# Kernel optimization log

Measured on AMD Instinct MI355X. Metric: run time of the kernel, lower is better.

The kernel has to match this reference:

```python
import jax, jax.numpy as jnp
import numpy as np

T, D, H, C, MAXLEN = 1024, 512, 512, 50257, 150


def setup_inputs() -> dict:
    key = jax.random.key(0)
    ks = iter(jax.random.split(key, 32))
    s = 0.1  # keep gates out of saturation
    def p(shape):
        return jax.random.normal(next(ks), shape, jnp.float32) * s
    return {
        "x": jax.random.normal(next(ks), (T, D), jnp.float32),
        "enc_Wih0": p((2, 4 * H, D)), "enc_Whh0": p((2, 4 * H, H)), "enc_b0": p((2, 4 * H)),
        "enc_Wih1": p((2, 4 * H, 2 * H)), "enc_Whh1": p((2, 4 * H, H)), "enc_b1": p((2, 4 * H)),
        "dec_Wih0": p((2, 4 * H, D)), "dec_Whh0": p((2, 4 * H, H)), "dec_b0": p((2, 4 * H)),
        "dec_Wih1": p((2, 4 * H, 2 * H)), "dec_Whh1": p((2, 4 * H, H)), "dec_b1": p((2, 4 * H)),
        "lin_W": p((C, 2 * H)), "lin_b": p((C,)),
        "emb": p((C, D)),
        "bos": p((D,)),
        "out_max_len": MAXLEN,
    }


def _cell(x, h, c, Wih, Whh, b):
    # PyTorch LSTM gate order: i, f, g, o; b = b_ih + b_hh
    g = Wih @ x + Whh @ h + b
    i, f, gg, o = jnp.split(g, 4)
    c = jax.nn.sigmoid(f) * c + jax.nn.sigmoid(i) * jnp.tanh(gg)
    h = jax.nn.sigmoid(o) * jnp.tanh(c)
    return h, c


def _run_dir(xs, Wih, Whh, b, reverse):
    Hh = Whh.shape[1]
    init = (jnp.zeros((Hh,), xs.dtype), jnp.zeros((Hh,), xs.dtype))
    def step(carry, xt):
        h, c = carry
        h, c = _cell(xt, h, c, Wih, Whh, b)
        return (h, c), h
    (hT, cT), hs = jax.lax.scan(step, init, xs, reverse=reverse)
    return hs, hT, cT  # hs aligned with input order


def _encode(x, layers):
    xs = x  # [T, D]
    h_fin, c_fin = [], []
    for (Wih, Whh, b) in layers:
        hs_f, hf, cf = _run_dir(xs, Wih[0], Whh[0], b[0], False)
        hs_b, hb, cb = _run_dir(xs, Wih[1], Whh[1], b[1], True)
        xs = jnp.concatenate([hs_f, hs_b], axis=-1)  # [T, 2H]
        h_fin.append(jnp.stack([hf, hb]))
        c_fin.append(jnp.stack([cf, cb]))
    return jnp.stack(h_fin), jnp.stack(c_fin)  # [L, 2, H]


def reference(x, enc_Wih0, enc_Whh0, enc_b0, enc_Wih1, enc_Whh1, enc_b1,
              dec_Wih0, dec_Whh0, dec_b0, dec_Wih1, dec_Whh1, dec_b1,
              lin_W, lin_b, emb, bos, out_max_len):
    layers_enc = [(enc_Wih0, enc_Whh0, enc_b0), (enc_Wih1, enc_Whh1, enc_b1)]
    layers_dec = [(dec_Wih0, dec_Whh0, dec_b0), (dec_Wih1, dec_Whh1, dec_b1)]

    h, c = _encode(x, layers_enc)  # [2, 2, H] each

    def dec_step(carry, _):
        buf, h, c = carry
        inp = buf
        nh, nc = [], []
        for l, (Wih, Whh, b) in enumerate(layers_dec):
            hf, cf = _cell(inp, h[l, 0], c[l, 0], Wih[0], Whh[0], b[0])
            hb, cb = _cell(inp, h[l, 1], c[l, 1], Wih[1], Whh[1], b[1])
            inp = jnp.concatenate([hf, hb])  # [2H]
            nh.append(jnp.stack([hf, hb]))
            nc.append(jnp.stack([cf, cb]))
        logits = lin_W @ inp + lin_b          # [C]
        tok = jnp.argmax(logits)              # greedy feedback
        buf = emb[tok]                        # [D]
        return (buf, jnp.stack(nh), jnp.stack(nc)), (logits, tok)

    _, (logits_seq, toks) = jax.lax.scan(dec_step, (bos, h, c), None, length=out_max_len)
    return logits_seq, toks  # [L_out, C], [L_out]
```

## Files before the change

### kernel.cpp

```cpp
#include <hip/hip_runtime.h>

typedef unsigned int u32;
typedef unsigned short u16;
typedef unsigned long long u64;

#define DEV static __device__ __forceinline__

DEV float sigf(float x){ return 1.0f / (1.0f + expf(-x)); }

DEV u64  ldA64(const u64* p){ return __hip_atomic_load(p, __ATOMIC_RELAXED, __HIP_MEMORY_SCOPE_AGENT); }
DEV void stA64(u64* p, u64 v){ __hip_atomic_store(p, v, __ATOMIC_RELAXED, __HIP_MEMORY_SCOPE_AGENT); }
DEV float ldAf(const float* p){ return __hip_atomic_load(p, __ATOMIC_RELAXED, __HIP_MEMORY_SCOPE_AGENT); }
DEV void stAf(float* p, float v){ __hip_atomic_store(p, v, __ATOMIC_RELAXED, __HIP_MEMORY_SCOPE_AGENT); }
DEV u32  ldA32(const u32* p){ return __hip_atomic_load(p, __ATOMIC_RELAXED, __HIP_MEMORY_SCOPE_AGENT); }

DEV u64 packHV(float h, u32 tag){ return (((u64)__float_as_uint(h)) << 32) | (u64)tag; }
DEV float unpackH(u64 v){ return __uint_as_float((u32)(v >> 32)); }

DEV u64 packKeyT(float v, u32 row, u32 tagv){
  u32 u = __float_as_uint(v);
  u = (u & 0x80000000u) ? ~u : (u | 0x80000000u);
  return (((u64)u) << 32) | ((u64)(0x1FFFFu - row) << 15) | (u64)tagv;
}
DEV float unpackKeyF(u64 k){
  u32 u = (u32)(k >> 32);
  u = (u & 0x80000000u) ? (u ^ 0x80000000u) : ~u;
  return __uint_as_float(u);
}

#if defined(__has_builtin)
#if __has_builtin(__builtin_amdgcn_sdot4)
#define HAVE_SDOT4 1
#endif
#endif
DEV int dot4i8(u32 a, u32 b, int acc){
#ifdef HAVE_SDOT4
  return __builtin_amdgcn_sdot4((int)a, (int)b, acc, false);
#else
  int s = acc;
  s += ((int)(a << 24) >> 24) * ((int)(b << 24) >> 24);
  s += ((int)(a << 16) >> 24) * ((int)(b << 16) >> 24);
  s += ((int)(a <<  8) >> 24) * ((int)(b <<  8) >> 24);
  s += ((int)(a      ) >> 24) * ((int)(b      ) >> 24);
  return s;
#endif
}

DEV int q8c(float v){ int q = (int)rintf(v); return q < -127 ? -127 : (q > 127 ? 127 : q); }
DEV u32 pk4(int a, int b, int c, int d){
  return (u32)(a & 255) | ((u32)(b & 255) << 8) | ((u32)(c & 255) << 16) | ((u32)(d & 255) << 24);
}

DEV float dotrow(const float4 A, const float4 B, const float4 Cc, const float4 D,
                 const float4 q0, const float4 q1, const float4 q2, const float4 q3){
  float s;
  s  = A.x*q0.x + A.y*q0.y + A.z*q0.z + A.w*q0.w;
  s += B.x*q1.x + B.y*q1.y + B.z*q1.z + B.w*q1.w;
  s += Cc.x*q2.x + Cc.y*q2.y + Cc.z*q2.z + Cc.w*q2.w;
  s += D.x*q3.x + D.y*q3.y + D.z*q3.z + D.w*q3.w;
  return s;
}

struct SM {
  float w1s[24576];
  float inpP[1600];
  float linp[1024];
  u32   qhp[256];
  float srow[200];
  float erow[200];
  float red[8];
  float dots[16];
  float cst0[4];
  float cst1[4];
  u64   wkey[4];
};

template<int CPT> DEV int pidx(int c){ int b = c / CPT; return b * (CPT + 4) + (c - b * CPT); }

template<int CPT, int DIN>
DEV void loadw(float* wreg, const float* Wih, const float* Whh, int jb4){
  const int tid = threadIdx.x, r = tid >> 4, p = tid & 15;
  const int R = 512 * (r >> 2) + jb4 + (r & 3);
  const float* s1 = Wih + (size_t)R * DIN;
  const float* s2 = Whh + (size_t)R * 512;
  #pragma unroll
  for (int k = 0; k < CPT; k += 4){
    const int col = p * CPT + k;
    const float4 v = *(const float4*)((col < DIN) ? (s1 + col) : (s2 + col - DIN));
    wreg[k] = v.x; wreg[k+1] = v.y; wreg[k+2] = v.z; wreg[k+3] = v.w;
  }
}

template<int CPT, int DIN, bool LOW>
DEV float dotp_reg(const float* wreg, const float* inpP, float acc){
  const int p = threadIdx.x & 15;
  const float* xi = inpP + p * (CPT + 4);
  #pragma unroll
  for (int k = 0; k < CPT; k += 4){
    const int col = p * CPT + k;
    if ((col < DIN) == LOW){
      const float4 xv = *(const float4*)(xi + k);
      acc = fmaf(wreg[k],   xv.x, acc);
      acc = fmaf(wreg[k+1], xv.y, acc);
      acc = fmaf(wreg[k+2], xv.z, acc);
      acc = fmaf(wreg[k+3], xv.w, acc);
    }
  }
  return acc;
}
DEV void dred16(float acc, float* dots){
  #pragma unroll
  for (int s = 1; s < 16; s <<= 1) acc += __shfl_xor(acc, s, 64);
  if ((threadIdx.x & 15) == 0) dots[threadIdx.x >> 4] = acc;
}

template<int CPT>
DEV void dot16(const float* wreg, const float* inpP, float* dots){
  const int tid = threadIdx.x, p = tid & 15;
  const float* xi = inpP + p * (CPT + 4);
  float acc = 0.f;
  #pragma unroll
  for (int k = 0; k < CPT; k += 4){
    const float4 xv = *(const float4*)(xi + k);
    acc = fmaf(wreg[k],   xv.x, acc);
    acc = fmaf(wreg[k+1], xv.y, acc);
    acc = fmaf(wreg[k+2], xv.z, acc);
    acc = fmaf(wreg[k+3], xv.w, acc);
  }
  dred16(acc, dots);
}

DEV void dot16_w1(const float* w1s, const float* inpP, float* dots){
  const int tid = threadIdx.x, p = tid & 15;
  const float* xi = inpP + p * 100;
  float acc = 0.f;
  #pragma unroll
  for (int k = 0; k < 96; k += 4){
    const float4 w4 = *(const float4*)(w1s + (k >> 2) * 1024 + tid * 4);
    const float4 xv = *(const float4*)(xi + k);
    acc = fmaf(w4.x, xv.x, acc);
    acc = fmaf(w4.y, xv.y, acc);
    acc = fmaf(w4.z, xv.z, acc);
    acc = fmaf(w4.w, xv.w, acc);
  }
  dred16(acc, dots);
}

DEV void gbar_phase(u32* g, u32 ev){
  __syncthreads();
  if (threadIdx.x == 0){
    __hip_atomic_fetch_add(g, 1u, __ATOMIC_RELEASE, __HIP_MEMORY_SCOPE_AGENT);
    const u32 tgt = 256u * ev;
    while (ldA32(g) < tgt) __builtin_amdgcn_s_sleep(8);
    (void)__hip_atomic_fetch_add(g, 0u, __ATOMIC_ACQUIRE, __HIP_MEMORY_SCOPE_AGENT);
    asm volatile("" ::: "memory");
  }
  __syncthreads();
}

DEV u64 exchange(u64* slots, u64 kwave , int w, u32 tagv, SM& sm){
  const int tid = threadIdx.x;
  if ((tid & 63) == 0) sm.wkey[tid >> 6] = kwave;
  __syncthreads();
  if (tid == 0){
    u64 k4 = sm.wkey[0];
    if (sm.wkey[1] > k4) k4 = sm.wkey[1];
    if (sm.wkey[2] > k4) k4 = sm.wkey[2];
    if (sm.wkey[3] > k4) k4 = sm.wkey[3];
    stA64(slots + (size_t)w * 16, k4);
  }
  __syncthreads();
  const u64* p = slots + (size_t)tid * 16;
  u64 kv = ldA64(p);
  while ((u32)(kv & 0x7FFFu) != tagv){ __builtin_amdgcn_s_sleep(1); kv = ldA64(p); }
  #pragma unroll
  for (int s = 1; s < 64; s <<= 1){
    const u64 o = (u64)__shfl_xor((unsigned long long)kv, s, 64);
    if (o > kv) kv = o;
  }
  if ((tid & 63) == 0) sm.wkey[tid >> 6] = kv;
  __syncthreads();
  u64 gk = sm.wkey[0];
  if (sm.wkey[1] > gk) gk = sm.wkey[1];
  if (sm.wkey[2] > gk) gk = sm.wkey[2];
  if (sm.wkey[3] > gk) gk = sm.wkey[3];
  return gk;
}

template<int DIN, bool WRITE_XS>
DEV void enc_layer(const float* __restrict__ xg, float* __restrict__ xs_out,
                   const float* __restrict__ Wih, const float* __restrict__ Whh,
                   const float* __restrict__ bias,
                   u64* __restrict__ ht, float* __restrict__ hfinL, float* __restrict__ cfinL,
                   const int dir, const int jb4, SM& sm)
{
  constexpr int CPT = (DIN + 512) / 16;
  constexpr int NX  = DIN / 256;
  const int tid = threadIdx.x;
  float wreg[CPT];
  loadw<CPT, DIN>(wreg, Wih + (size_t)dir * 2048 * DIN, Whh + (size_t)dir * 2048 * 512, jb4);
  float b_i = 0.f, b_f = 0.f, b_g = 0.f, b_o = 0.f;
  if (tid < 4){
    const int j = jb4 + tid;
    sm.cst0[tid] = 0.f;
    b_i = bias[dir*2048 +        j];
    b_f = bias[dir*2048 +  512 + j];
    b_g = bias[dir*2048 + 1024 + j];
    b_o = bias[dir*2048 + 1536 + j];
  }
  float xr[NX];
  {
    const int t0 = dir ? 1023 : 0;
    #pragma unroll
    for (int i = 0; i < NX; ++i){
      const int c = tid + 256 * i;
      xr[i] = (DIN == 512) ? xg[(size_t)t0 * DIN + c] : ldAf(xg + (size_t)t0 * DIN + c);
    }
  }
  for (int step = 0; step < 1024; ++step){
    #pragma unroll
    for (int i = 0; i < NX; ++i) sm.inpP[pidx<CPT>(tid + 256 * i)] = xr[i];
    __syncthreads();
    const u64* hp = ht + (step & 1) * 512;
    const u32 want = (u32)step;
    u64 a = ldA64(hp + tid*2);
    u64 b = ldA64(hp + tid*2 + 1);
    float acc = dotp_reg<CPT, DIN, true>(wreg, sm.inpP, 0.f);
    while ((u32)a != want){ __builtin_amdgcn_s_sleep(1); a = ldA64(hp + tid*2); }
    while ((u32)b != want){ __builtin_amdgcn_s_sleep(1); b = ldA64(hp + tid*2 + 1); }
    sm.inpP[pidx<CPT>(DIN + tid*2)]     = unpackH(a);
    sm.inpP[pidx<CPT>(DIN + tid*2 + 1)] = unpackH(b);
    __syncthreads();
    if (step < 1023){
      const int tn = dir ? (1022 - step) : (step + 1);
      #pragma unroll
      for (int i = 0; i < NX; ++i){
        const int c = tid + 256 * i;
        xr[i] = (DIN == 512) ? xg[(size_t)tn * DIN + c] : ldAf(xg + (size_t)tn * DIN + c);
      }
    }
    acc = dotp_reg<CPT, DIN, false>(wreg, sm.inpP, acc);
    dred16(acc, sm.dots);
    __syncthreads();
    if (tid < 4){
      const float gi = sm.dots[tid]      + b_i;
      const float gf = sm.dots[4 + tid]  + b_f;
      const float gg = sm.dots[8 + tid]  + b_g;
      const float go = sm.dots[12 + tid] + b_o;
      const float cc = sigf(gf) * sm.cst0[tid] + sigf(gi) * tanhf(gg);
      const float hh = sigf(go) * tanhf(cc);
      sm.cst0[tid] = cc;
      const int t = dir ? (1023 - step) : step;
      const int j = jb4 + tid;
      stA64(ht + ((step + 1) & 1) * 512 + j, packHV(hh, (u32)(step + 1)));
      if (WRITE_XS) stAf(xs_out + (size_t)t * 1024 + dir * 512 + j, hh);
      if (step == 1023){ stAf(hfinL + dir*512 + j, hh); stAf(cfinL + dir*512 + j, cc); }
    }
  }
}

__global__ void bilstm_init(u32* ws){
  for (u32 i = threadIdx.x; i < 49152u; i += 256u) ws[i] = 0u;
}

__global__ void cvt_q8(const float* __restrict__ w, uint4* __restrict__ q8,
                       float* __restrict__ meta, const int C){
  const int wv = threadIdx.x >> 6, lane = threadIdx.x & 63;
  const int stride = gridDim.x * 4;
  for (int r = blockIdx.x * 4 + wv; r < C; r += stride){
    const float4* src = (const float4*)(w + (size_t)r * 1024) + lane * 4;
    const float4 v0 = src[0], v1 = src[1], v2 = src[2], v3 = src[3];
    float m = fmaxf(fmaxf(fmaxf(fabsf(v0.x), fabsf(v0.y)), fmaxf(fabsf(v0.z), fabsf(v0.w))),
                    fmaxf(fmaxf(fabsf(v1.x), fabsf(v1.y)), fmaxf(fabsf(v1.z), fabsf(v1.w))));
    m = fmaxf(m, fmaxf(fmaxf(fabsf(v2.x), fabsf(v2.y)), fmaxf(fabsf(v2.z), fabsf(v2.w))));
    m = fmaxf(m, fmaxf(fmaxf(fabsf(v3.x), fabsf(v3.y)), fmaxf(fabsf(v3.z), fabsf(v3.w))));
    #pragma unroll
    for (int s = 1; s < 64; s <<= 1) m = fmaxf(m, __shfl_xor(m, s, 64));
    const float inv = (m > 1e-30f) ? (127.0f / m) : 0.0f;
    const float sw = m * (1.0f / 127.0f);
    const int qa0 = q8c(v0.x*inv), qa1 = q8c(v0.y*inv), qa2 = q8c(v0.z*inv), qa3 = q8c(v0.w*inv);
    const int qb0 = q8c(v1.x*inv), qb1 = q8c(v1.y*inv), qb2 = q8c(v1.z*inv), qb3 = q8c(v1.w*inv);
    const int qc0 = q8c(v2.x*inv), qc1 = q8c(v2.y*inv), qc2 = q8c(v2.z*inv), qc3 = q8c(v2.w*inv);
    const int qd0 = q8c(v3.x*inv), qd1 = q8c(v3.y*inv), qd2 = q8c(v3.z*inv), qd3 = q8c(v3.w*inv);
    uint4 st;
    st.x = pk4(qa0,qa1,qa2,qa3); st.y = pk4(qb0,qb1,qb2,qb3);
    st.z = pk4(qc0,qc1,qc2,qc3); st.w = pk4(qd0,qd1,qd2,qd3);
    q8[(size_t)r * 64 + lane] = st;
    float sq = (float)(abs(qa0)+abs(qa1)+abs(qa2)+abs(qa3)+abs(qb0)+abs(qb1)+abs(qb2)+abs(qb3)
                     + abs(qc0)+abs(qc1)+abs(qc2)+abs(qc3)+abs(qd0)+abs(qd1)+abs(qd2)+abs(qd3));
    #pragma unroll
    for (int s = 1; s < 64; s <<= 1) sq += __shfl_xor(sq, s, 64);
    if (lane == 0){ meta[2*r] = sw; meta[2*r+1] = sq; }
  }
}

template<int LINQ8>
__global__ __launch_bounds__(256, 1)
void bilstm_persist(const float* __restrict__ x,
                    const float* __restrict__ eW0, const float* __restrict__ eU0, const float* __restrict__ eb0,
                    const float* __restrict__ eW1, const float* __restrict__ eU1, const float* __restrict__ eb1,
                    const float* __restrict__ dW0, const float* __restrict__ dU0, const float* __restrict__ db0,
                    const float* __restrict__ dW1, const float* __restrict__ dU1, const float* __restrict__ db1,
                    const float* __restrict__ linW, const float* __restrict__ linb,
                    const float* __restrict__ emb, const float* __restrict__ bos,
                    float* __restrict__ out, float* __restrict__ ws, const int L, const int C)
{
  __shared__ SM sm;
  const int w = blockIdx.x;
  const int tid = threadIdx.x;
  const int dir = (w >> 2) & 1;
  const int jb4 = ((w >> 3) * 4 + (w & 3)) * 4;

  u64*  htagE = (u64*)ws;
  u64*  h0t   = htagE + 4096;
  u64*  h1t   = h0t + 2048;
  float* hfin = (float*)(h1t + 2048);
  float* cfin = hfin + 2048;
  u32*  gbar  = (u32*)(cfin + 2048);
  u64*  gkeyA = (u64*)((char*)ws + 131072);
  u64*  gkeyB = (u64*)((char*)ws + 163840);
  const float* meta = (const float*)((const char*)ws + 196608);
  const uint4* q8u  = (const uint4*)((const char*)ws + 602112);
  float* xs1  = out;

  enc_layer<512,  true >(x,   xs1,     eW0, eU0, eb0, htagE + (0*2 + dir)*1024, hfin,        cfin,        dir, jb4, sm);
  gbar_phase(gbar, 1);
  enc_layer<1024, false>(xs1, nullptr, eW1, eU1, eb1, htagE + (1*2 + dir)*1024, hfin + 1024, cfin + 1024, dir, jb4, sm);
  gbar_phase(gbar, 2);

  float w0reg[64];
  loadw<64, 512>(w0reg, dW0 + (size_t)dir*2048*512, dU0 + (size_t)dir*2048*512, jb4);
  {
    const int r = tid >> 4, p = tid & 15;
    const int R = 512 * (r >> 2) + jb4 + (r & 3);
    const float* s1 = dW1 + (size_t)dir*2048*1024 + (size_t)R * 1024;
    const float* s2 = dU1 + (size_t)dir*2048*512  + (size_t)R * 512;
    #pragma unroll
    for (int k = 0; k < 96; k += 4){
      const int col = p * 96 + k;
      const float4 v = *(const float4*)((col < 1024) ? (s1 + col) : (s2 + col - 1024));
      *(float4*)(sm.w1s + (k >> 2) * 1024 + tid * 4) = v;
    }
  }

  float b0i=0,b0f=0,b0g=0,b0o=0, b1i=0,b1f=0,b1g=0,b1o=0;
  if (tid < 4){
    const int j = jb4 + tid;
    sm.cst0[tid] = ldAf(&cfin[dir*512 + j]);
    sm.cst1[tid] = ldAf(&cfin[1024 + dir*512 + j]);
    b0i = db0[dir*2048 + j];        b0f = db0[dir*2048 + 512 + j];
    b0g = db0[dir*2048 + 1024 + j]; b0o = db0[dir*2048 + 1536 + j];
    b1i = db1[dir*2048 + j];        b1f = db1[dir*2048 + 512 + j];
    b1g = db1[dir*2048 + 1024 + j]; b1o = db1[dir*2048 + 1536 + j];
  }
  const int rbase = w * 196 + (w < 81 ? w : 81);
  const int rn    = 196 + (w < 81 ? 1 : 0);
  int tok = 0;

  for (int t = 0; t < L; ++t){
    {
      const float* src = (t == 0) ? bos : (emb + (size_t)tok * 512);
      sm.inpP[pidx<64>(tid)]       = src[tid];
      sm.inpP[pidx<64>(tid + 256)] = src[tid + 256];
      if (t == 0){
        sm.inpP[pidx<64>(512 + tid*2)]     = ldAf(&hfin[dir*512 + tid*2]);
        sm.inpP[pidx<64>(512 + tid*2 + 1)] = ldAf(&hfin[dir*512 + tid*2 + 1]);
      } else {
        const u64* hp = h0t + (dir*2 + ((t-1) & 1)) * 512;
        const u32 want = (u32)t;
        u64 a = ldA64(hp + tid*2), b = ldA64(hp + tid*2 + 1);
        while ((u32)a != want){ __builtin_amdgcn_s_sleep(1); a = ldA64(hp + tid*2); }
        while ((u32)b != want){ __builtin_amdgcn_s_sleep(1); b = ldA64(hp + tid*2 + 1); }
        sm.inpP[pidx<64>(512 + tid*2)]     = unpackH(a);
        sm.inpP[pidx<64>(512 + tid*2 + 1)] = unpackH(b);
      }
      __syncthreads();
      dot16<64>(w0reg, sm.inpP, sm.dots);
      __syncthreads();
      if (tid < 4){
        const float gi = sm.dots[tid] + b0i, gf = sm.dots[4+tid] + b0f;
        const float gg = sm.dots[8+tid] + b0g, go = sm.dots[12+tid] + b0o;
        const float cc = sigf(gf) * sm.cst0[tid] + sigf(gi) * tanhf(gg);
        const float hh = sigf(go) * tanhf(cc);
        sm.cst0[tid] = cc;
        stA64(h0t + (dir*2 + (t & 1))*512 + jb4 + tid, packHV(hh, (u32)(t + 1)));
      }
      __syncthreads();
    }

    {
      const u32 want = (u32)(t + 1);
      #pragma unroll
      for (int i = 0; i < 4; ++i){
        const int c = tid + 256 * i;
        const int d = c >> 9, idx = c & 511;
        const u64* hp = h0t + (d*2 + (t & 1)) * 512 + idx;
        u64 v = ldA64(hp);
        while ((u32)v != want){ __builtin_amdgcn_s_sleep(1); v = ldA64(hp); }
        sm.inpP[pidx<96>(c)] = unpackH(v);
      }
      if (t == 0){
        sm.inpP[pidx<96>(1024 + tid*2)]     = ldAf(&hfin[1024 + dir*512 + tid*2]);
        sm.inpP[pidx<96>(1024 + tid*2 + 1)] = ldAf(&hfin[1024 + dir*512 + tid*2 + 1]);
      } else {
        const u64* hq = h1t + (dir*2 + ((t-1) & 1)) * 512;
        const u32 want1 = (u32)t;
        u64 e = ldA64(hq + tid*2), f = ldA64(hq + tid*2 + 1);
        while ((u32)e != want1){ __builtin_amdgcn_s_sleep(1); e = ldA64(hq + tid*2); }
        while ((u32)f != want1){ __builtin_amdgcn_s_sleep(1); f = ldA64(hq + tid*2 + 1); }
        sm.inpP[pidx<96>(1024 + tid*2)]     = unpackH(e);
        sm.inpP[pidx<96>(1024 + tid*2 + 1)] = unpackH(f);
      }
      __syncthreads();
      dot16_w1(sm.w1s, sm.inpP, sm.dots);
      __syncthreads();
      if (tid < 4){
        const float gi = sm.dots[tid] + b1i, gf = sm.dots[4+tid] + b1f;
        const float gg = sm.dots[8+tid] + b1g, go = sm.dots[12+tid] + b1o;
        const float cc = sigf(gf) * sm.cst1[tid] + sigf(gi) * tanhf(gg);
        const float hh = sigf(go) * tanhf(cc);
        sm.cst1[tid] = cc;
        stA64(h1t + (dir*2 + (t & 1))*512 + jb4 + tid, packHV(hh, (u32)(t + 1)));
      }
    }

    const int wv = tid >> 6, lane = tid & 63;
    {
      const u32 want = (u32)(t + 1);
      float pm = 0.f;
      #pragma unroll
      for (int i = 0; i < 4; ++i){
        const int c = tid + 256 * i;
        const int d = c >> 9, idx = c & 511;
        const u64* hp = h1t + (d*2 + (t & 1)) * 512 + idx;
        u64 v = ldA64(hp);
        while ((u32)v != want){ __builtin_amdgcn_s_sleep(1); v = ldA64(hp); }
        const float hv = unpackH(v);
        sm.linp[c] = hv;
        pm = fmaxf(pm, fabsf(hv));
      }

      if constexpr (LINQ8){
        #pragma unroll
        for (int s = 1; s < 64; s <<= 1) pm = fmaxf(pm, __shfl_xor(pm, s, 64));
        if (lane == 0) sm.red[wv] = pm;
        __syncthreads();
        const float maxh = fmaxf(fmaxf(sm.red[0], sm.red[1]), fmaxf(sm.red[2], sm.red[3]));
        const float inv_sh = (maxh > 1e-30f) ? (127.0f / maxh) : 0.0f;
        const float sh = maxh * (1.0f / 127.0f);
        {
          const float4 hv = *(const float4*)(sm.linp + 4 * tid);
          const int q0 = q8c(hv.x * inv_sh), q1 = q8c(hv.y * inv_sh);
          const int q2 = q8c(hv.z * inv_sh), q3 = q8c(hv.w * inv_sh);
          sm.qhp[tid] = pk4(q0, q1, q2, q3);
          float sq = (float)(abs(q0) + abs(q1) + abs(q2) + abs(q3));
          #pragma unroll
          for (int s = 1; s < 64; s <<= 1) sq += __shfl_xor(sq, s, 64);
          if (lane == 0) sm.red[4 + wv] = sq;
        }
        __syncthreads();
        const float Sqh = sm.red[4] + sm.red[5] + sm.red[6] + sm.red[7];
        const u32 qh0 = sm.qhp[lane*4], qh1 = sm.qhp[lane*4+1];
        const u32 qh2 = sm.qhp[lane*4+2], qh3 = sm.qhp[lane*4+3];
        float lb = -3.0e38f;
        for (int i0 = wv; i0 < rn; i0 += 16){
          const int ia = i0;
          const int ib = (i0+4  > rn-1) ? rn-1 : i0+4;
          const int ic = (i0+8  > rn-1) ? rn-1 : i0+8;
          const int id = (i0+12 > rn-1) ? rn-1 : i0+12;
          const int ra = rbase+ia, rb = rbase+ib, rc = rbase+ic, rd = rbase+id;
          const float2 Ma = *(const float2*)(meta + 2*ra);
          const float2 Mb = *(const float2*)(meta + 2*rb);
          const float2 Mc = *(const float2*)(meta + 2*rc);
          const float2 Md = *(const float2*)(meta + 2*rd);
          const uint4 wa = q8u[(size_t)ra*64 + lane];
          const uint4 wb = q8u[(size_t)rb*64 + lane];
          const uint4 wc = q8u[(size_t)rc*64 + lane];
          const uint4 wd = q8u[(size_t)rd*64 + lane];
          int da = dot4i8(wa.x,qh0, dot4i8(wa.y,qh1, dot4i8(wa.z,qh2, dot4i8(wa.w,qh3, 0))));
          int db = dot4i8(wb.x,qh0, dot4i8(wb.y,qh1, dot4i8(wb.z,qh2, dot4i8(wb.w,qh3, 0))));
          int dc = dot4i8(wc.x,qh0, dot4i8(wc.y,qh1, dot4i8(wc.z,qh2, dot4i8(wc.w,qh3, 0))));
          int dd = dot4i8(wd.x,qh0, dot4i8(wd.y,qh1, dot4i8(wd.z,qh2, dot4i8(wd.w,qh3, 0))));
          #pragma unroll
          for (int s = 1; s < 64; s <<= 1){
            da += __shfl_xor(da, s, 64);
            db += __shfl_xor(db, s, 64);
            dc += __shfl_xor(dc, s, 64);
            dd += __shfl_xor(dd, s, 64);
          }
          if (lane == 0){
            const float ca = Ma.x * sh, cb = Mb.x * sh, cc2 = Mc.x * sh, cd = Md.x * sh;
            const float sa = ca * (float)da + linb[ra];
            const float sb = cb * (float)db + linb[rb];
            const float sc = cc2 * (float)dc + linb[rc];
            const float sd = cd * (float)dd + linb[rd];
            const float ea = ca * (0.5f*(Ma.y + Sqh) + 256.0f) * 1.0002f + 1e-4f;
            const float eb = cb * (0.5f*(Mb.y + Sqh) + 256.0f) * 1.0002f + 1e-4f;
            const float ec = cc2 * (0.5f*(Mc.y + Sqh) + 256.0f) * 1.0002f + 1e-4f;
            const float ed = cd * (0.5f*(Md.y + Sqh) + 256.0f) * 1.0002f + 1e-4f;
            out[(size_t)t*C + ra] = sa; out[(size_t)t*C + rb] = sb;
            out[(size_t)t*C + rc] = sc; out[(size_t)t*C + rd] = sd;
            sm.srow[ia] = sa; sm.erow[ia] = ea;
            sm.srow[ib] = sb; sm.erow[ib] = eb;
            sm.srow[ic] = sc; sm.erow[ic] = ec;
            sm.srow[id] = sd; sm.erow[id] = ed;
            lb = fmaxf(lb, sa - ea); lb = fmaxf(lb, sb - eb);
            lb = fmaxf(lb, sc - ec); lb = fmaxf(lb, sd - ed);
          }
        }
        const u64 gkA = exchange(gkeyA, packKeyT(lb, 0u, (u32)(t+1)), w, (u32)(t+1), sm);
        const float Lb = unpackKeyF(gkA);
        u64 kwB = packKeyT(-3.0e38f, 0x1FFFFu, (u32)(t+1));
        const float4* ip4 = (const float4*)(sm.linp + lane * 16);
        const float4 q0f = ip4[0], q1f = ip4[1], q2f = ip4[2], q3f = ip4[3];
        for (int i = wv; i < rn; i += 4){
          if (sm.srow[i] + sm.erow[i] >= Lb){
            const int row = rbase + i;
            const float4* wp = (const float4*)(linW + (size_t)row * 1024) + lane * 4;
            float s = dotrow(wp[0], wp[1], wp[2], wp[3], q0f, q1f, q2f, q3f);
            #pragma unroll
            for (int sh2 = 1; sh2 < 64; sh2 <<= 1) s += __shfl_xor(s, sh2, 64);
            if (lane == 0){
              s += linb[row];
              const u64 k = packKeyT(s, (u32)row, (u32)(t+1));
              if (k > kwB) kwB = k;
            }
          }
        }
        const u64 gkB = exchange(gkeyB, kwB, w, (u32)(t+1), sm);
        tok = (int)(0x1FFFFu - ((u32)(gkB >> 15) & 0x1FFFFu));
        if (w == 0 && tid == 0) out[(size_t)L * C + t] = (float)tok;
      } else {
        __syncthreads();
        const float4* ip4 = (const float4*)(sm.linp + lane * 16);
        const float4 q0 = ip4[0], q1 = ip4[1], q2 = ip4[2], q3 = ip4[3];
        u64 kmax = packKeyT(-3.0e38f, 0x1FFFFu, (u32)(t+1));
        const int rmaxr = rbase + rn - 1;
        for (int i0 = wv; i0 < rn; i0 += 16){
          const int ra = rbase + i0;
          const int rb = (ra + 4  > rmaxr) ? rmaxr : ra + 4;
          const int rc = (ra + 8  > rmaxr) ? rmaxr : ra + 8;
          const int rd = (ra + 12 > rmaxr) ? rmaxr : ra + 12;
          const float ba = linb[ra], bb = linb[rb], bc = linb[rc], bd = linb[rd];
          const float4* pa = (const float4*)(linW + (size_t)ra * 1024) + lane * 4;
          const float4* pb = (const float4*)(linW + (size_t)rb * 1024) + lane * 4;
          const float4* pc = (const float4*)(linW + (size_t)rc * 1024) + lane * 4;
          const float4* pd = (const float4*)(linW + (size_t)rd * 1024) + lane * 4;
          float sa = dotrow(pa[0],pa[1],pa[2],pa[3], q0,q1,q2,q3);
          float sb = dotrow(pb[0],pb[1],pb[2],pb[3], q0,q1,q2,q3);
          float sc = dotrow(pc[0],pc[1],pc[2],pc[3], q0,q1,q2,q3);
          float sd = dotrow(pd[0],pd[1],pd[2],pd[3], q0,q1,q2,q3);
          #pragma unroll
          for (int sh = 1; sh < 64; sh <<= 1){
            sa += __shfl_xor(sa, sh, 64);
            sb += __shfl_xor(sb, sh, 64);
            sc += __shfl_xor(sc, sh, 64);
            sd += __shfl_xor(sd, sh, 64);
          }
          if (lane == 0){
            sa += ba; sb += bb; sc += bc; sd += bd;
            out[(size_t)t * C + ra] = sa;
            out[(size_t)t * C + rb] = sb;
            out[(size_t)t * C + rc] = sc;
            out[(size_t)t * C + rd] = sd;
            u64 k;
            k = packKeyT(sa, (u32)ra, (u32)(t+1)); if (k > kmax) kmax = k;
            k = packKeyT(sb, (u32)rb, (u32)(t+1)); if (k > kmax) kmax = k;
            k = packKeyT(sc, (u32)rc, (u32)(t+1)); if (k > kmax) kmax = k;
            k = packKeyT(sd, (u32)rd, (u32)(t+1)); if (k > kmax) kmax = k;
          }
        }
        const u64 gkB = exchange(gkeyB, kmax, w, (u32)(t+1), sm);
        tok = (int)(0x1FFFFu - ((u32)(gkB >> 15) & 0x1FFFFu));
        if (w == 0 && tid == 0) out[(size_t)L * C + t] = (float)tok;
      }
    }
  }
}

extern "C" void kernel_launch(void* const* d_in, const int* in_sizes, int n_in,
                              void* d_out, int out_size, void* d_ws, size_t ws_size,
                              hipStream_t stream)
{
  const float* x    = (const float*)d_in[0];
  const float* eW0  = (const float*)d_in[1];
  const float* eU0  = (const float*)d_in[2];
  const float* eb0  = (const float*)d_in[3];
  const float* eW1  = (const float*)d_in[4];
  const float* eU1  = (const float*)d_in[5];
  const float* eb1  = (const float*)d_in[6];
  const float* dW0  = (const float*)d_in[7];
  const float* dU0  = (const float*)d_in[8];
  const float* db0  = (const float*)d_in[9];
  const float* dW1  = (const float*)d_in[10];
  const float* dU1  = (const float*)d_in[11];
  const float* db1  = (const float*)d_in[12];
  const float* linW = (const float*)d_in[13];
  const float* linb = (const float*)d_in[14];
  const float* emb  = (const float*)d_in[15];
  const float* bos  = (const float*)d_in[16];

  const int C = in_sizes[14];
  const int L = out_size / (C + 1);

  const size_t need = 602112 + (size_t)C * 1024;
  const bool q8 = (ws_size >= need);

  hipLaunchKernelGGL(bilstm_init, dim3(1), dim3(256), 0, stream, (u32*)d_ws);
  if (q8){
    hipLaunchKernelGGL(cvt_q8, dim3(2048), dim3(256), 0, stream,
                       linW, (uint4*)((char*)d_ws + 602112),
                       (float*)((char*)d_ws + 196608), C);
    hipLaunchKernelGGL((bilstm_persist<1>), dim3(256), dim3(256), 0, stream,
                       x, eW0, eU0, eb0, eW1, eU1, eb1,
                       dW0, dU0, db0, dW1, dU1, db1,
                       linW, linb, emb, bos,
                       (float*)d_out, (float*)d_ws, L, C);
  } else {
    hipLaunchKernelGGL((bilstm_persist<0>), dim3(256), dim3(256), 0, stream,
                       x, eW0, eU0, eb0, eW1, eU1, eb1,
                       dW0, dU0, db0, dW1, dU1, db1,
                       linW, linb, emb, bos,
                       (float*)d_out, (float*)d_ws, L, C);
  }
}
```

Measured before the change: 10.37 ms.

## Replace global lower-bound exchange with block-local bound and batch int8 row loads

Drops the grid-wide atomic exchange of the int8 lower bound and computes the pruning threshold per block from a shared-memory reduction. Each block then rescores only rows whose upper bound reaches its own local bound, which removes one cross-block synchronisation per decode step. A local bound is weaker than the global one, so more rows may be rescored in fp32. The int8 scoring loop also issues 16 row loads per wave before reducing, to expose more memory parallelism at the cost of more registers.

```diff
diff --git a/kernel.cpp b/kernel.cpp
--- a/kernel.cpp
+++ b/kernel.cpp
@@ -21,11 +21,6 @@
   u32 u = __float_as_uint(v);
   u = (u & 0x80000000u) ? ~u : (u | 0x80000000u);
   return (((u64)u) << 32) | ((u64)(0x1FFFFu - row) << 15) | (u64)tagv;
-}
-DEV float unpackKeyF(u64 k){
-  u32 u = (u32)(k >> 32);
-  u = (u & 0x80000000u) ? (u ^ 0x80000000u) : ~u;
-  return __uint_as_float(u);
 }
 
 #if defined(__has_builtin)
@@ -68,7 +63,7 @@
   u32   qhp[256];
   float srow[200];
   float erow[200];
-  float red[8];
+  float red[12];
   float dots[16];
   float cst0[4];
   float cst1[4];
@@ -158,7 +153,7 @@
   __syncthreads();
 }
 
-DEV u64 exchange(u64* slots, u64 kwave , int w, u32 tagv, SM& sm){
+DEV u64 exchange(u64* slots, u64 kwave, int w, u32 tagv, SM& sm){
   const int tid = threadIdx.x;
   if ((tid & 63) == 0) sm.wkey[tid >> 6] = kwave;
   __syncthreads();
@@ -317,7 +312,6 @@
   float* hfin = (float*)(h1t + 2048);
   float* cfin = hfin + 2048;
   u32*  gbar  = (u32*)(cfin + 2048);
-  u64*  gkeyA = (u64*)((char*)ws + 131072);
   u64*  gkeyB = (u64*)((char*)ws + 163840);
   const float* meta = (const float*)((const char*)ws + 196608);
   const uint4* q8u  = (const uint4*)((const char*)ws + 602112);
@@ -358,6 +352,7 @@
   int tok = 0;
 
   for (int t = 0; t < L; ++t){
+    const u32 tag = (u32)(t + 1);
     {
       const float* src = (t == 0) ? bos : (emb + (size_t)tok * 512);
       sm.inpP[pidx<64>(tid)]       = src[tid];
@@ -383,20 +378,19 @@
         const float cc = sigf(gf) * sm.cst0[tid] + sigf(gi) * tanhf(gg);
         const float hh = sigf(go) * tanhf(cc);
         sm.cst0[tid] = cc;
-        stA64(h0t + (dir*2 + (t & 1))*512 + jb4 + tid, packHV(hh, (u32)(t + 1)));
+        stA64(h0t + (dir*2 + (t & 1))*512 + jb4 + tid, packHV(hh, tag));
       }
       __syncthreads();
     }
 
     {
-      const u32 want = (u32)(t + 1);
       #pragma unroll
       for (int i = 0; i < 4; ++i){
         const int c = tid + 256 * i;
         const int d = c >> 9, idx = c & 511;
         const u64* hp = h0t + (d*2 + (t & 1)) * 512 + idx;
         u64 v = ldA64(hp);
-        while ((u32)v != want){ __builtin_amdgcn_s_sleep(1); v = ldA64(hp); }
+        while ((u32)v != tag){ __builtin_amdgcn_s_sleep(1); v = ldA64(hp); }
         sm.inpP[pidx<96>(c)] = unpackH(v);
       }
       if (t == 0){
@@ -420,13 +414,12 @@
         const float cc = sigf(gf) * sm.cst1[tid] + sigf(gi) * tanhf(gg);
         const float hh = sigf(go) * tanhf(cc);
         sm.cst1[tid] = cc;
-        stA64(h1t + (dir*2 + (t & 1))*512 + jb4 + tid, packHV(hh, (u32)(t + 1)));
+        stA64(h1t + (dir*2 + (t & 1))*512 + jb4 + tid, packHV(hh, tag));
       }
     }
 
     const int wv = tid >> 6, lane = tid & 63;
     {
-      const u32 want = (u32)(t + 1);
       float pm = 0.f;
       #pragma unroll
       for (int i = 0; i < 4; ++i){
@@ -434,7 +427,7 @@
         const int d = c >> 9, idx = c & 511;
         const u64* hp = h1t + (d*2 + (t & 1)) * 512 + idx;
         u64 v = ldA64(hp);
-        while ((u32)v != want){ __builtin_amdgcn_s_sleep(1); v = ldA64(hp); }
+        while ((u32)v != tag){ __builtin_amdgcn_s_sleep(1); v = ldA64(hp); }
         const float hv = unpackH(v);
         sm.linp[c] = hv;
         pm = fmaxf(pm, fabsf(hv));
@@ -447,7 +440,7 @@
         __syncthreads();
         const float maxh = fmaxf(fmaxf(sm.red[0], sm.red[1]), fmaxf(sm.red[2], sm.red[3]));
         const float inv_sh = (maxh > 1e-30f) ? (127.0f / maxh) : 0.0f;
-        const float sh = maxh * (1.0f / 127.0f);
+        const float shs = maxh * (1.0f / 127.0f);
         {
           const float4 hv = *(const float4*)(sm.linp + 4 * tid);
           const int q0 = q8c(hv.x * inv_sh), q1 = q8c(hv.y * inv_sh);
@@ -463,54 +456,42 @@
         const u32 qh0 = sm.qhp[lane*4], qh1 = sm.qhp[lane*4+1];
         const u32 qh2 = sm.qhp[lane*4+2], qh3 = sm.qhp[lane*4+3];
         float lb = -3.0e38f;
-        for (int i0 = wv; i0 < rn; i0 += 16){
-          const int ia = i0;
-          const int ib = (i0+4  > rn-1) ? rn-1 : i0+4;
-          const int ic = (i0+8  > rn-1) ? rn-1 : i0+8;
-          const int id = (i0+12 > rn-1) ? rn-1 : i0+12;
-          const int ra = rbase+ia, rb = rbase+ib, rc = rbase+ic, rd = rbase+id;
-          const float2 Ma = *(const float2*)(meta + 2*ra);
-          const float2 Mb = *(const float2*)(meta + 2*rb);
-          const float2 Mc = *(const float2*)(meta + 2*rc);
-          const float2 Md = *(const float2*)(meta + 2*rd);
-          const uint4 wa = q8u[(size_t)ra*64 + lane];
-          const uint4 wb = q8u[(size_t)rb*64 + lane];
-          const uint4 wc = q8u[(size_t)rc*64 + lane];
-          const uint4 wd = q8u[(size_t)rd*64 + lane];
-          int da = dot4i8(wa.x,qh0, dot4i8(wa.y,qh1, dot4i8(wa.z,qh2, dot4i8(wa.w,qh3, 0))));
-          int db = dot4i8(wb.x,qh0, dot4i8(wb.y,qh1, dot4i8(wb.z,qh2, dot4i8(wb.w,qh3, 0))));
-          int dc = dot4i8(wc.x,qh0, dot4i8(wc.y,qh1, dot4i8(wc.z,qh2, dot4i8(wc.w,qh3, 0))));
-          int dd = dot4i8(wd.x,qh0, dot4i8(wd.y,qh1, dot4i8(wd.z,qh2, dot4i8(wd.w,qh3, 0))));
+        for (int i0 = wv; i0 < rn; i0 += 64){
+          int idx[16];
+          uint4 wq[16];
+          #pragma unroll
+          for (int j = 0; j < 16; ++j){
+            int i = i0 + 4 * j; if (i > rn - 1) i = rn - 1;
+            idx[j] = i;
+            wq[j] = q8u[(size_t)(rbase + i) * 64 + lane];
+          }
+          int d[16];
+          #pragma unroll
+          for (int j = 0; j < 16; ++j)
+            d[j] = dot4i8(wq[j].x, qh0, dot4i8(wq[j].y, qh1, dot4i8(wq[j].z, qh2, dot4i8(wq[j].w, qh3, 0))));
           #pragma unroll
           for (int s = 1; s < 64; s <<= 1){
-            da += __shfl_xor(da, s, 64);
-            db += __shfl_xor(db, s, 64);
-            dc += __shfl_xor(dc, s, 64);
-            dd += __shfl_xor(dd, s, 64);
+            #pragma unroll
+            for (int j = 0; j < 16; ++j) d[j] += __shfl_xor(d[j], s, 64);
           }
           if (lane == 0){
-            const float ca = Ma.x * sh, cb = Mb.x * sh, cc2 = Mc.x * sh, cd = Md.x * sh;
-            const float sa = ca * (float)da + linb[ra];
-            const float sb = cb * (float)db + linb[rb];
-            const float sc = cc2 * (float)dc + linb[rc];
-            const float sd = cd * (float)dd + linb[rd];
-            const float ea = ca * (0.5f*(Ma.y + Sqh) + 256.0f) * 1.0002f + 1e-4f;
-            const float eb = cb * (0.5f*(Mb.y + Sqh) + 256.0f) * 1.0002f + 1e-4f;
-            const float ec = cc2 * (0.5f*(Mc.y + Sqh) + 256.0f) * 1.0002f + 1e-4f;
-            const float ed = cd * (0.5f*(Md.y + Sqh) + 256.0f) * 1.0002f + 1e-4f;
-            out[(size_t)t*C + ra] = sa; out[(size_t)t*C + rb] = sb;
-            out[(size_t)t*C + rc] = sc; out[(size_t)t*C + rd] = sd;
-            sm.srow[ia] = sa; sm.erow[ia] = ea;
-            sm.srow[ib] = sb; sm.erow[ib] = eb;
-            sm.srow[ic] = sc; sm.erow[ic] = ec;
-            sm.srow[id] = sd; sm.erow[id] = ed;
-            lb = fmaxf(lb, sa - ea); lb = fmaxf(lb, sb - eb);
-            lb = fmaxf(lb, sc - ec); lb = fmaxf(lb, sd - ed);
+            #pragma unroll
+            for (int j = 0; j < 16; ++j){
+              const int i = idx[j], row = rbase + i;
+              const float2 M = *(const float2*)(meta + 2 * row);
+              const float csc = M.x * shs;
+              const float sv = csc * (float)d[j] + linb[row];
+              const float ev = csc * (0.5f * (M.y + Sqh) + 256.0f) * 1.0002f + 1e-4f;
+              out[(size_t)t * C + row] = sv;
+              sm.srow[i] = sv; sm.erow[i] = ev;
+              lb = fmaxf(lb, sv - ev);
+            }
           }
         }
-        const u64 gkA = exchange(gkeyA, packKeyT(lb, 0u, (u32)(t+1)), w, (u32)(t+1), sm);
-        const float Lb = unpackKeyF(gkA);
-        u64 kwB = packKeyT(-3.0e38f, 0x1FFFFu, (u32)(t+1));
+        if (lane == 0) sm.red[8 + wv] = lb;
+        __syncthreads();
+        const float Lb = fmaxf(fmaxf(sm.red[8], sm.red[9]), fmaxf(sm.red[10], sm.red[11]));
+        u64 kwB = packKeyT(-3.0e38f, 0x1FFFFu, tag);
         const float4* ip4 = (const float4*)(sm.linp + lane * 16);
         const float4 q0f = ip4[0], q1f = ip4[1], q2f = ip4[2], q3f = ip4[3];
         for (int i = wv; i < rn; i += 4){
@@ -522,19 +503,19 @@
             for (int sh2 = 1; sh2 < 64; sh2 <<= 1) s += __shfl_xor(s, sh2, 64);
             if (lane == 0){
               s += linb[row];
-              const u64 k = packKeyT(s, (u32)row, (u32)(t+1));
+              const u64 k = packKeyT(s, (u32)row, tag);
               if (k > kwB) kwB = k;
             }
           }
         }
-        const u64 gkB = exchange(gkeyB, kwB, w, (u32)(t+1), sm);
+        const u64 gkB = exchange(gkeyB, kwB, w, tag, sm);
         tok = (int)(0x1FFFFu - ((u32)(gkB >> 15) & 0x1FFFFu));
         if (w == 0 && tid == 0) out[(size_t)L * C + t] = (float)tok;
       } else {
         __syncthreads();
         const float4* ip4 = (const float4*)(sm.linp + lane * 16);
         const float4 q0 = ip4[0], q1 = ip4[1], q2 = ip4[2], q3 = ip4[3];
-        u64 kmax = packKeyT(-3.0e38f, 0x1FFFFu, (u32)(t+1));
+        u64 kmax = packKeyT(-3.0e38f, 0x1FFFFu, tag);
         const int rmaxr = rbase + rn - 1;
         for (int i0 = wv; i0 < rn; i0 += 16){
           const int ra = rbase + i0;
@@ -564,13 +545,13 @@
             out[(size_t)t * C + rc] = sc;
             out[(size_t)t * C + rd] = sd;
             u64 k;
-            k = packKeyT(sa, (u32)ra, (u32)(t+1)); if (k > kmax) kmax = k;
-            k = packKeyT(sb, (u32)rb, (u32)(t+1)); if (k > kmax) kmax = k;
-            k = packKeyT(sc, (u32)rc, (u32)(t+1)); if (k > kmax) kmax = k;
-            k = packKeyT(sd, (u32)rd, (u32)(t+1)); if (k > kmax) kmax = k;
+            k = packKeyT(sa, (u32)ra, tag); if (k > kmax) kmax = k;
+            k = packKeyT(sb, (u32)rb, tag); if (k > kmax) kmax = k;
+            k = packKeyT(sc, (u32)rc, tag); if (k > kmax) kmax = k;
+            k = packKeyT(sd, (u32)rd, tag); if (k > kmax) kmax = k;
           }
         }
-        const u64 gkB = exchange(gkeyB, kmax, w, (u32)(t+1), sm);
+        const u64 gkB = exchange(gkeyB, kmax, w, tag, sm);
         tok = (int)(0x1FFFFu - ((u32)(gkB >> 15) & 0x1FFFFu));
         if (w == 0 && tid == 0) out[(size_t)L * C + t] = (float)tok;
       }
```

New measurement: 12.71 ms. 1.23x slower.
